# Optimization experiments

Measured on AMD Instinct MI355X. Metric: run time of the kernel, lower is better.

## Reference

```python
import jax, jax.numpy as jnp
import numpy as np

B, D, CLASSES = 8192, 128, 5

def setup_inputs() -> dict:
    key = jax.random.key(0)
    ks = jax.random.split(key, 7)
    d2 = 2 * D
    return {
        "left": jax.random.normal(ks[0], (B, D), jnp.float32),
        "right": jax.random.normal(ks[1], (B, D), jnp.float32),
        "V": jax.random.normal(ks[2], (d2, d2, D), jnp.float32) * 0.02,
        "W_w": jax.random.normal(ks[3], (D, d2), jnp.float32) * 0.02,
        "W_b": jax.random.normal(ks[4], (D,), jnp.float32) * 0.02,
        "Ws_w": jax.random.normal(ks[5], (CLASSES, D), jnp.float32) * 0.02,
        "Ws_b": jax.random.normal(ks[6], (CLASSES,), jnp.float32) * 0.02,
    }

def reference(left, right, V, W_w, W_b, Ws_w, Ws_b):
    # phrase: [B, 2d]
    phrase = jnp.concatenate([left, right], axis=1)
    d2 = phrase.shape[1]
    d = V.shape[2]
    # Fused bilinear tensor product: result[b,k] = sum_ij phrase[b,i] V[i,j,k] phrase[b,j]
    # One GEMM: (B,2d) @ (2d, 2d*d) -> (B,2d,d), then contract j with phrase.
    pv = (phrase @ V.reshape(d2, d2 * d)).reshape(-1, d2, d)   # [B,2d,d]
    tp = jnp.einsum('bj,bjk->bk', phrase, pv)                  # [B,d]
    # node: tanh(tensorProduct + W(phrase))
    h = jnp.tanh(tp + phrase @ W_w.T + W_b)                    # [B,d]
    # sentiment: log_softmax(Ws(h))
    logits = h @ Ws_w.T + Ws_b                                 # [B,classes]
    return jax.nn.log_softmax(logits, axis=1)
```

## Files before the change

### kernel.cpp

```cpp
#include <hip/hip_runtime.h>
#include <hip/hip_fp16.h>
#include <math.h>

typedef _Float16 f16x8 __attribute__((ext_vector_type(8)));
typedef _Float16 f16x4 __attribute__((ext_vector_type(4)));
typedef float f32x4 __attribute__((ext_vector_type(4)));

#define DD     128
#define D2     256
#define NB     8192
#define NCLS   5
#define KSPLIT 8
#define BM     128
#define PPAD   258
#define NSB    36
#define SB_BYTES  262144u
#define TAIL_OFF  (36u * 262144u)
#define PART_OFF  (10u * 1048576u)

__global__ void prep_vt(const float* __restrict__ V, const float* __restrict__ Ww,
                        _Float16* __restrict__ Vt) {
    int t = blockIdx.x * 256 + threadIdx.x;
    int u = t >> 7;
    int n = t & 127;
    f16x8 v;
    if (u < NSB * 128) {
        int s = u >> 7, g = u & 127;
        int bi = 0, rem = s;
        while (rem >= 8 - bi) { rem -= 8 - bi; ++bi; }
        int bj = bi + rem;
        int i  = bi * 32 + (g >> 2);
        int j0 = bj * 32 + (g & 3) * 8;
        if (bi == bj) {
            #pragma unroll
            for (int e = 0; e < 8; ++e)
                v[e] = (_Float16)V[((size_t)i * 256 + j0 + e) * 128 + n];
        } else {
            #pragma unroll
            for (int e = 0; e < 8; ++e)
                v[e] = (_Float16)(V[((size_t)i * 256 + j0 + e) * 128 + n]
                                + V[((size_t)(j0 + e) * 256 + i) * 128 + n]);
        }
    } else {
        int g = u - NSB * 128;
        int j0 = g * 8;
        #pragma unroll
        for (int e = 0; e < 8; ++e)
            v[e] = (_Float16)Ww[n * D2 + j0 + e];
    }
    *(f16x8*)(Vt + (size_t)u * 1024 + n * 8) = v;
}

__global__ __launch_bounds__(256, 2) void gemm_bilinear(
        const float* __restrict__ left, const float* __restrict__ right,
        const _Float16* __restrict__ Vt, float* __restrict__ part) {
    __shared__ _Float16 P[BM][PPAD];

    const int bid = blockIdx.x;
    const int ks  = bid & 7;
    const int m0  = (bid >> 3) * BM;
    const int tid = threadIdx.x;

    for (int it = 0; it < 32; ++it) {
        int f4  = it * 256 + tid;
        int row = f4 >> 6;
        int col = (f4 & 63) * 4;
        const float* src = (col < DD) ? (left  + (size_t)(m0 + row) * DD + col)
                                      : (right + (size_t)(m0 + row) * DD + (col - DD));
        float4 x = *(const float4*)src;
        f16x4 hv;
        hv[0] = (_Float16)x.x; hv[1] = (_Float16)x.y;
        hv[2] = (_Float16)x.z; hv[3] = (_Float16)x.w;
        *(f16x4*)&P[row][col] = hv;
    }
    __syncthreads();

    const int lane = tid & 63;
    const int wid  = tid >> 6;
    const int wm   = wid >> 1, wn = wid & 1;
    const int l15  = lane & 15, lg = lane >> 4;
    const int rowb = wm * 64;
    const int coln = wn * 64;

    f32x4 acc[4][4];
    #pragma unroll
    for (int u = 0; u < 4; ++u)
        #pragma unroll
        for (int w = 0; w < 4; ++w)
            acc[u][w] = (f32x4){0.f, 0.f, 0.f, 0.f};

    const unsigned lane_nbyte = (unsigned)((coln + l15) * 16);
    #define LDV(off) (*(const f16x8*)((const char*)Vt + (off)))

    #define LOADB(BUF)                                                                    \
        asm volatile("global_load_dwordx4 %0, %4, %5\n\t"                                 \
                     "global_load_dwordx4 %1, %4, %5 offset:256\n\t"                      \
                     "global_load_dwordx4 %2, %4, %5 offset:512\n\t"                      \
                     "global_load_dwordx4 %3, %4, %5 offset:768"                          \
            : "=&v"(BUF[0]), "=&v"(BUF[1]), "=&v"(BUF[2]), "=&v"(BUF[3])                  \
            : "v"(voff), "s"(Vt));                                                        \
        voff += 8192u;

    #define WAITN(N, BUF)                                                                 \
        asm volatile("s_waitcnt vmcnt(" #N ")"                                            \
            : "+v"(BUF[0]), "+v"(BUF[1]), "+v"(BUF[2]), "+v"(BUF[3]));

    #define MFMA_CLUSTER(BUF, IBE)                                                        \
        _Pragma("unroll")                                                                 \
        for (int mr = 0; mr < 4; ++mr) {                                                  \
            const _Float16 sc = pis[mr][IBE];                                             \
            const f16x8 a = pj[mr] * sc;                                                  \
            _Pragma("unroll")                                                             \
            for (int nr = 0; nr < 4; ++nr)                                                \
                acc[mr][nr] = __builtin_amdgcn_mfma_f32_16x16x32_f16(a, BUF[nr], acc[mr][nr], 0, 0, 0); \
        }

    #define LOAD_PIS(IBC)                                                                 \
        f16x8 pis[4];                                                                     \
        _Pragma("unroll")                                                                 \
        for (int mr = 0; mr < 4; ++mr)                                                    \
            pis[mr] = *(const f16x8*)&P[rowb + mr * 16 + l15][bi * 32 + (IBC) * 8];

    #pragma unroll 1
    for (int si = 0; si < 5; ++si) {
        int s, ibcS, ibcE;
        if (si < 4) { s = ks * 4 + si;      ibcS = 0;            ibcE = 4; }
        else        { s = 32 + (ks >> 1);   ibcS = (ks & 1) * 2; ibcE = ibcS + 2; }

        int bi = 0, rem = s;
        while (rem >= 8 - bi) { rem -= 8 - bi; ++bi; }
        const int bj = bi + rem;

        f16x8 pj[4];
        #pragma unroll
        for (int mr = 0; mr < 4; ++mr)
            pj[mr] = *(const f16x8*)&P[rowb + mr * 16 + l15][bj * 32 + lg * 8];

        unsigned voff = lane_nbyte + (unsigned)s * SB_BYTES + (unsigned)(lg * 2048)
                      + (unsigned)(ibcS * 65536);

        f16x8 B0[4], B1[4], B2[4], B3[4];
        LOADB(B0)
        LOADB(B1)

        #pragma unroll 1
        for (int ibc = ibcS; ibc < ibcE - 1; ++ibc) {
            LOAD_PIS(ibc)
            LOADB(B2)  WAITN(8, B0)  MFMA_CLUSTER(B0, 0)
            LOADB(B3)  WAITN(8, B1)  MFMA_CLUSTER(B1, 1)
            LOADB(B0)  WAITN(8, B2)  MFMA_CLUSTER(B2, 2)
            LOADB(B1)  WAITN(8, B3)  MFMA_CLUSTER(B3, 3)
            LOADB(B2)  WAITN(8, B0)  MFMA_CLUSTER(B0, 4)
            LOADB(B3)  WAITN(8, B1)  MFMA_CLUSTER(B1, 5)
            LOADB(B0)  WAITN(8, B2)  MFMA_CLUSTER(B2, 6)
            LOADB(B1)  WAITN(8, B3)  MFMA_CLUSTER(B3, 7)
        }

        {
            LOAD_PIS(ibcE - 1)
            LOADB(B2)  WAITN(8, B0)  MFMA_CLUSTER(B0, 0)
            LOADB(B3)  WAITN(8, B1)  MFMA_CLUSTER(B1, 1)
            LOADB(B0)  WAITN(8, B2)  MFMA_CLUSTER(B2, 2)
            LOADB(B1)  WAITN(8, B3)  MFMA_CLUSTER(B3, 3)
            LOADB(B2)  WAITN(8, B0)  MFMA_CLUSTER(B0, 4)
            LOADB(B3)  WAITN(8, B1)  MFMA_CLUSTER(B1, 5)
                       WAITN(4, B2)  MFMA_CLUSTER(B2, 6)
                       WAITN(0, B3)  MFMA_CLUSTER(B3, 7)
        }
    }

    if (ks == KSPLIT - 1) {
        #pragma unroll 1
        for (int jc = 0; jc < 8; ++jc) {
            unsigned voff = TAIL_OFF + (unsigned)((jc * 4 + lg) * 2048) + lane_nbyte;
            f16x8 bfr[4];
            #pragma unroll
            for (int nr = 0; nr < 4; ++nr) bfr[nr] = LDV(voff + nr * 256);
            #pragma unroll
            for (int mr = 0; mr < 4; ++mr) {
                const f16x8 a = *(const f16x8*)&P[rowb + mr * 16 + l15][jc * 32 + lg * 8];
                #pragma unroll
                for (int nr = 0; nr < 4; ++nr)
                    acc[mr][nr] = __builtin_amdgcn_mfma_f32_16x16x32_f16(a, bfr[nr], acc[mr][nr], 0, 0, 0);
            }
        }
    }

    float* base = part + ((size_t)ks * NB + m0) * DD;
    #pragma unroll
    for (int mr = 0; mr < 4; ++mr)
        #pragma unroll
        for (int nr = 0; nr < 4; ++nr) {
            const int col = coln + nr * 16 + l15;
            #pragma unroll
            for (int q = 0; q < 4; ++q) {
                const int row = rowb + mr * 16 + lg * 4 + q;
                base[(size_t)row * DD + col] = acc[mr][nr][q];
            }
        }
}

__global__ void finish(const float* __restrict__ part, const float* __restrict__ Wb,
                       const float* __restrict__ Wsw, const float* __restrict__ Wsb,
                       float* __restrict__ out) {
    int t  = blockIdx.x * 256 + threadIdx.x;
    int b  = t >> 3;
    int kq = t & 7;
    if (b >= NB) return;
    float lg[NCLS];
    #pragma unroll
    for (int c = 0; c < NCLS; ++c) lg[c] = 0.f;

    const float* pb = part + (size_t)b * DD + kq * 16;
    #pragma unroll 1
    for (int k4 = 0; k4 < 4; ++k4) {
        float4 tt = *(const float4*)(Wb + kq * 16 + k4 * 4);
        #pragma unroll
        for (int s = 0; s < KSPLIT; ++s) {
            float4 p = *(const float4*)(pb + (size_t)s * NB * DD + k4 * 4);
            tt.x += p.x; tt.y += p.y; tt.z += p.z; tt.w += p.w;
        }
        float tq[4] = {tt.x, tt.y, tt.z, tt.w};
        #pragma unroll
        for (int q = 0; q < 4; ++q) {
            float h = tanhf(tq[q]);
            int k = kq * 16 + k4 * 4 + q;
            #pragma unroll
            for (int c = 0; c < NCLS; ++c)
                lg[c] += h * Wsw[c * DD + k];
        }
    }
    #pragma unroll
    for (int c = 0; c < NCLS; ++c) {
        lg[c] += __shfl_xor(lg[c], 1);
        lg[c] += __shfl_xor(lg[c], 2);
        lg[c] += __shfl_xor(lg[c], 4);
    }
    if (kq == 0) {
        #pragma unroll
        for (int c = 0; c < NCLS; ++c) lg[c] += Wsb[c];
        float mx = lg[0];
        #pragma unroll
        for (int c = 1; c < NCLS; ++c) mx = fmaxf(mx, lg[c]);
        float sum = 0.f;
        #pragma unroll
        for (int c = 0; c < NCLS; ++c) sum += expf(lg[c] - mx);
        float lse = logf(sum);
        #pragma unroll
        for (int c = 0; c < NCLS; ++c) out[b * NCLS + c] = lg[c] - mx - lse;
    }
}

extern "C" void kernel_launch(void* const* d_in, const int* in_sizes, int n_in,
                              void* d_out, int out_size, void* d_ws, size_t ws_size,
                              hipStream_t stream) {
    const float* left  = (const float*)d_in[0];
    const float* right = (const float*)d_in[1];
    const float* V     = (const float*)d_in[2];
    const float* Ww    = (const float*)d_in[3];
    const float* Wb    = (const float*)d_in[4];
    const float* Wsw   = (const float*)d_in[5];
    const float* Wsb   = (const float*)d_in[6];
    float* out = (float*)d_out;

    _Float16* Vt = (_Float16*)d_ws;
    float* part  = (float*)((char*)d_ws + PART_OFF);

    hipLaunchKernelGGL(prep_vt, dim3(2320), dim3(256), 0, stream, V, Ww, Vt);
    hipLaunchKernelGGL(gemm_bilinear, dim3((NB / BM) * KSPLIT), dim3(256), 0, stream,
                       left, right, Vt, part);
    hipLaunchKernelGGL(finish, dim3(NB * 8 / 256), dim3(256), 0, stream, part, Wb, Wsw, Wsb, out);
}
```

Baseline: 97.69 us.

## Store split-K partials in fp16 and spread linear-term tail across all splits

The split-K partial sums are now written as fp16 instead of fp32, which halves the write traffic in the GEMM kernel and the read traffic in the finish kernel. The W(phrase) tail chunk, which previously ran entirely in the last split, is now spread so each split handles one of its 8 chunks, balancing work across blocks. The finish kernel reads each row's 16 values per split with vectorized fp16 loads and reduces them in fp32. Rounding partials to fp16 adds precision error before tanh.

```diff
diff --git a/kernel.cpp b/kernel.cpp
--- a/kernel.cpp
+++ b/kernel.cpp
@@ -53,7 +53,7 @@
 
 __global__ __launch_bounds__(256, 2) void gemm_bilinear(
         const float* __restrict__ left, const float* __restrict__ right,
-        const _Float16* __restrict__ Vt, float* __restrict__ part) {
+        const _Float16* __restrict__ Vt, _Float16* __restrict__ part) {
     __shared__ _Float16 P[BM][PPAD];
 
     const int bid = blockIdx.x;
@@ -169,24 +169,22 @@
         }
     }
 
-    if (ks == KSPLIT - 1) {
-        #pragma unroll 1
-        for (int jc = 0; jc < 8; ++jc) {
-            unsigned voff = TAIL_OFF + (unsigned)((jc * 4 + lg) * 2048) + lane_nbyte;
-            f16x8 bfr[4];
-            #pragma unroll
-            for (int nr = 0; nr < 4; ++nr) bfr[nr] = LDV(voff + nr * 256);
-            #pragma unroll
-            for (int mr = 0; mr < 4; ++mr) {
-                const f16x8 a = *(const f16x8*)&P[rowb + mr * 16 + l15][jc * 32 + lg * 8];
-                #pragma unroll
-                for (int nr = 0; nr < 4; ++nr)
-                    acc[mr][nr] = __builtin_amdgcn_mfma_f32_16x16x32_f16(a, bfr[nr], acc[mr][nr], 0, 0, 0);
-            }
-        }
-    }
-
-    float* base = part + ((size_t)ks * NB + m0) * DD;
+    {
+        const int jc = ks;
+        unsigned voff = TAIL_OFF + (unsigned)((jc * 4 + lg) * 2048) + lane_nbyte;
+        f16x8 bfr[4];
+        #pragma unroll
+        for (int nr = 0; nr < 4; ++nr) bfr[nr] = LDV(voff + nr * 256);
+        #pragma unroll
+        for (int mr = 0; mr < 4; ++mr) {
+            const f16x8 a = *(const f16x8*)&P[rowb + mr * 16 + l15][jc * 32 + lg * 8];
+            #pragma unroll
+            for (int nr = 0; nr < 4; ++nr)
+                acc[mr][nr] = __builtin_amdgcn_mfma_f32_16x16x32_f16(a, bfr[nr], acc[mr][nr], 0, 0, 0);
+        }
+    }
+
+    _Float16* base = part + ((size_t)ks * NB + m0) * DD;
     #pragma unroll
     for (int mr = 0; mr < 4; ++mr)
         #pragma unroll
@@ -195,40 +193,43 @@
             #pragma unroll
             for (int q = 0; q < 4; ++q) {
                 const int row = rowb + mr * 16 + lg * 4 + q;
-                base[(size_t)row * DD + col] = acc[mr][nr][q];
+                base[(size_t)row * DD + col] = (_Float16)acc[mr][nr][q];
             }
         }
 }
 
-__global__ void finish(const float* __restrict__ part, const float* __restrict__ Wb,
+__global__ void finish(const _Float16* __restrict__ part, const float* __restrict__ Wb,
                        const float* __restrict__ Wsw, const float* __restrict__ Wsb,
                        float* __restrict__ out) {
     int t  = blockIdx.x * 256 + threadIdx.x;
     int b  = t >> 3;
     int kq = t & 7;
     if (b >= NB) return;
+
+    float sum[16];
+    #pragma unroll
+    for (int q = 0; q < 16; ++q) sum[q] = Wb[kq * 16 + q];
+
+    const _Float16* pb = part + (size_t)b * DD + kq * 16;
+    #pragma unroll
+    for (int s = 0; s < KSPLIT; ++s) {
+        const _Float16* ps = pb + (size_t)s * NB * DD;
+        f16x8 v0 = *(const f16x8*)(ps);
+        f16x8 v1 = *(const f16x8*)(ps + 8);
+        #pragma unroll
+        for (int e = 0; e < 8; ++e) { sum[e] += (float)v0[e]; sum[8 + e] += (float)v1[e]; }
+    }
+
     float lg[NCLS];
     #pragma unroll
     for (int c = 0; c < NCLS; ++c) lg[c] = 0.f;
-
-    const float* pb = part + (size_t)b * DD + kq * 16;
-    #pragma unroll 1
-    for (int k4 = 0; k4 < 4; ++k4) {
-        float4 tt = *(const float4*)(Wb + kq * 16 + k4 * 4);
-        #pragma unroll
-        for (int s = 0; s < KSPLIT; ++s) {
-            float4 p = *(const float4*)(pb + (size_t)s * NB * DD + k4 * 4);
-            tt.x += p.x; tt.y += p.y; tt.z += p.z; tt.w += p.w;
-        }
-        float tq[4] = {tt.x, tt.y, tt.z, tt.w};
-        #pragma unroll
-        for (int q = 0; q < 4; ++q) {
-            float h = tanhf(tq[q]);
-            int k = kq * 16 + k4 * 4 + q;
-            #pragma unroll
-            for (int c = 0; c < NCLS; ++c)
-                lg[c] += h * Wsw[c * DD + k];
-        }
+    #pragma unroll
+    for (int q = 0; q < 16; ++q) {
+        float h = tanhf(sum[q]);
+        int k = kq * 16 + q;
+        #pragma unroll
+        for (int c = 0; c < NCLS; ++c)
+            lg[c] += h * Wsw[c * DD + k];
     }
     #pragma unroll
     for (int c = 0; c < NCLS; ++c) {
@@ -242,10 +243,10 @@
         float mx = lg[0];
         #pragma unroll
         for (int c = 1; c < NCLS; ++c) mx = fmaxf(mx, lg[c]);
-        float sum = 0.f;
-        #pragma unroll
-        for (int c = 0; c < NCLS; ++c) sum += expf(lg[c] - mx);
-        float lse = logf(sum);
+        float s = 0.f;
+        #pragma unroll
+        for (int c = 0; c < NCLS; ++c) s += expf(lg[c] - mx);
+        float lse = logf(s);
         #pragma unroll
         for (int c = 0; c < NCLS; ++c) out[b * NCLS + c] = lg[c] - mx - lse;
     }
@@ -263,8 +264,8 @@
     const float* Wsb   = (const float*)d_in[6];
     float* out = (float*)d_out;
 
-    _Float16* Vt = (_Float16*)d_ws;
-    float* part  = (float*)((char*)d_ws + PART_OFF);
+    _Float16* Vt   = (_Float16*)d_ws;
+    _Float16* part = (_Float16*)((char*)d_ws + PART_OFF);
 
     hipLaunchKernelGGL(prep_vt, dim3(2320), dim3(256), 0, stream, V, Ww, Vt);
     hipLaunchKernelGGL(gemm_bilinear, dim3((NB / BM) * KSPLIT), dim3(256), 0, stream,
```

Measured after the change: 91.37 us. 6.5% less time.
